# Kernel optimization log

Measured on AMD Instinct MI355X. Metric: run time of the kernel, lower is better.

## Reference

```python
import jax, jax.numpy as jnp
import numpy as np

HIDDEN = 64
FORECAST = 30
B, T = 4096, 1024


def setup_inputs() -> dict:
    key = jax.random.key(0)
    ks = jax.random.split(key, 7)
    s = 1.0 / np.sqrt(HIDDEN)  # torch LSTM/Linear uniform init scale
    u = lambda k, shape: jax.random.uniform(k, shape, jnp.float32, -s, s)
    return {
        "x": jax.random.normal(ks[0], (B, T, 1), jnp.float32),
        "W_ih": u(ks[1], (4 * HIDDEN, 1)),      # gates order: i, f, g, o (torch)
        "W_hh": u(ks[2], (4 * HIDDEN, HIDDEN)),
        "b_ih": u(ks[3], (4 * HIDDEN,)),
        "b_hh": u(ks[4], (4 * HIDDEN,)),
        "fc_W": u(ks[5], (FORECAST, HIDDEN)),
        "fc_b": u(ks[6], (FORECAST,)),
    }


def _lstm_last_hidden(x, W_ih, W_hh, b_ih, b_hh):
    # Precompute input contributions for all timesteps: [B, T, 4H]
    xg = jnp.einsum("bti,gi->btg", x, W_ih) + b_ih + b_hh
    H = W_hh.shape[1]
    W_hh_T = W_hh.T  # [H, 4H]

    def step(carry, xt):  # xt: [B, 4H]
        h, c = carry
        gates = xt + h @ W_hh_T
        i, f, g, o = jnp.split(gates, 4, axis=-1)
        i = jax.nn.sigmoid(i)
        f = jax.nn.sigmoid(f)
        g = jnp.tanh(g)
        o = jax.nn.sigmoid(o)
        c = f * c + i * g
        h = o * jnp.tanh(c)
        return (h, c), None

    Bsz = x.shape[0]
    h0 = jnp.zeros((Bsz, H), x.dtype)
    c0 = jnp.zeros((Bsz, H), x.dtype)
    (h_last, _), _ = jax.lax.scan(step, (h0, c0), jnp.swapaxes(xg, 0, 1))
    return h_last  # [B, H]


def reference(x, W_ih, W_hh, b_ih, b_hh, fc_W, fc_b):
    h_last = _lstm_last_hidden(x, W_ih, W_hh, b_ih, b_hh)
    return h_last @ fc_W.T + fc_b  # [B, FORECAST]
```

## Files before the change

kernel.cpp:

```cpp
#include <hip/hip_runtime.h>
#include <math.h>

#define T_STEPS 1024
#define FORECAST 30

typedef __attribute__((ext_vector_type(8))) _Float16 half8;
typedef __attribute__((ext_vector_type(2))) _Float16 half2v;
typedef __attribute__((ext_vector_type(4))) float f32x4;
typedef __attribute__((ext_vector_type(2))) float f32x2;

__device__ __forceinline__ float rcp_fast(float v){ return __builtin_amdgcn_rcpf(v); }
__device__ __forceinline__ float exp2_fast(float v){ return __builtin_amdgcn_exp2f(v); }
__device__ __forceinline__ f32x4 mfma16(half8 a, half8 b, f32x4 c){
    return __builtin_amdgcn_mfma_f32_16x16x32_f16(a, b, c, 0, 0, 0);
}
__device__ __forceinline__ half2v pack_f16(float a, float b){
    return __builtin_bit_cast(half2v, __builtin_amdgcn_cvt_pkrtz(a, b));
}

__global__ __launch_bounds__(512, 1)
void lstm_mfma_kernel(const float* __restrict__ x,
                      const float* __restrict__ W_ih,
                      const float* __restrict__ W_hh,
                      const float* __restrict__ b_ih,
                      const float* __restrict__ b_hh,
                      const float* __restrict__ fc_W,
                      const float* __restrict__ fc_b,
                      float* __restrict__ out)
{
    __shared__ __align__(16) _Float16 hs[2][16][64];
    __shared__ float xs[2][64][16];

    const int tid = threadIdx.x;
    const int l   = tid & 63;
    const int w   = tid >> 6;
    const int l15 = l & 15;
    const int l4  = l >> 4;
    const int bb  = blockIdx.x * 16;

    const float L2E  = 1.44269504088896f;
    const float TL2E = 2.88539008177793f;

    const int   ga   = l15 & 3;
    const float Srow = (ga == 2) ? TL2E : -L2E;
    half8 A[2][2];
    #pragma unroll
    for (int T = 0; T < 2; ++T) {
        const int gc = ga*64 + w*8 + T*4 + (l15 >> 2);
        #pragma unroll
        for (int kc = 0; kc < 2; ++kc) {
            #pragma unroll
            for (int e = 0; e < 8; ++e) {
                const int p   = kc*32 + l4*8 + e;
                const int jin = (p & ~7) + ((p & 1) << 2) + ((p & 7) >> 1);
                A[T][kc][e] = (_Float16)(W_hh[gc*64 + jin] * Srow);
            }
        }
    }

    float wih[2][4], bia[2][4];
    #pragma unroll
    for (int T = 0; T < 2; ++T) {
        const int jT = w*8 + T*4 + l4;
        #pragma unroll
        for (int r = 0; r < 4; ++r) {
            const float S = (r == 2) ? TL2E : -L2E;
            const int   g = r*64 + jT;
            wih[T][r] = W_ih[g] * S;
            bia[T][r] = (b_ih[g] + b_hh[g]) * S;
        }
    }

    const int rbase = (l15*128 + l4*16) ^ ((l15&7)<<4);
    const int hwoff = (l15*128 + w*16 + l4*4) ^ ((l15&7)<<4);
    char* const buf0 = (char*)hs;
    char* const buf1 = (char*)hs + 2048;

    #pragma unroll
    for (int it = 0; it < 2; ++it) {
        const int b = w*2 + it;
        xs[0][l][b] = x[(long long)(bb + b)*T_STEPS + l];
    }
    ((unsigned*)hs)[512 + tid] = 0u;
    __syncthreads();

    f32x2 cc = {0.f, 0.f}, hh01 = {0.f, 0.f};
    float xv = xs[0][0][l15];

    #define LSTM_STEP(T_CUR, RBUF, WBUF)                                        \
    {                                                                           \
        const int t_ = (T_CUR);                                                 \
        const half8 b0 = *(const half8*)((RBUF) + rbase);                       \
        const half8 b1 = *(const half8*)((RBUF) + (rbase ^ 64));                \
        f32x4 acc0, acc1;                                                       \
        _Pragma("unroll")                                                       \
        for (int r = 0; r < 4; ++r) {                                           \
            acc0[r] = fmaf(xv, wih[0][r], bia[0][r]);                           \
            acc1[r] = fmaf(xv, wih[1][r], bia[1][r]);                           \
        }                                                                       \
        acc0 = mfma16(A[0][0], b0, acc0);                                       \
        acc1 = mfma16(A[1][0], b0, acc1);                                       \
        acc0 = mfma16(A[0][1], b1, acc0);                                       \
        acc1 = mfma16(A[1][1], b1, acc1);                                       \
        const int t1_ = t_ + 1;                                                 \
        const float xvn = xs[(t1_ >> 6) & 1][t1_ & 63][l15];                    \
        f32x2 eI, eF, eG, eO;                                                   \
        eI[0] = exp2_fast(acc0[0]); eI[1] = exp2_fast(acc1[0]);                 \
        eF[0] = exp2_fast(acc0[1]); eF[1] = exp2_fast(acc1[1]);                 \
        eG[0] = exp2_fast(acc0[2]); eG[1] = exp2_fast(acc1[2]);                 \
        eO[0] = exp2_fast(acc0[3]); eO[1] = exp2_fast(acc1[3]);                 \
        const f32x2 u  = eI + 1.0f;                                             \
        const f32x2 v  = eF + 1.0f;                                             \
        const f32x2 s  = eG + 1.0f;                                             \
        const f32x2 m  = s - 2.0f;                                              \
        const f32x2 us = u * s;                                                 \
        const f32x2 vm = v * m;                                                 \
        const f32x2 N  = cc * us + vm;                                          \
        const f32x2 Dd = us * v;                                                \
        f32x2 rD; rD[0] = rcp_fast(Dd[0]); rD[1] = rcp_fast(Dd[1]);             \
        cc = N * rD;                                                            \
        f32x2 a2 = cc * TL2E;                                                   \
        a2[0] = fminf(a2[0], 80.f); a2[1] = fminf(a2[1], 80.f);                 \
        const f32x2 oD = eO + 1.0f;                                             \
        f32x2 Tt; Tt[0] = exp2_fast(a2[0]); Tt[1] = exp2_fast(a2[1]);           \
        const f32x2 Dh = oD * (Tt + 1.0f);                                      \
        f32x2 rH; rH[0] = rcp_fast(Dh[0]); rH[1] = rcp_fast(Dh[1]);             \
        hh01 = (Tt - 1.0f) * rH;                                                \
        *(half2v*)((WBUF) + hwoff) = pack_f16(hh01[0], hh01[1]);                \
        xv = xvn;                                                               \
        __syncthreads();                                                        \
    }

    for (int t2 = 0; t2 < T_STEPS; t2 += 2) {
        if ((t2 & 63) == 0 && t2 + 64 < T_STEPS) {
            #pragma unroll
            for (int it = 0; it < 2; ++it) {
                const int b = w*2 + it;
                xs[(((t2 >> 6) & 1)) ^ 1][l][b] =
                    x[(long long)(bb + b)*T_STEPS + t2 + 64 + l];
            }
        }
        LSTM_STEP(t2,     buf1, buf0);
        LSTM_STEP(t2 + 1, buf0, buf1);
    }
    #undef LSTM_STEP

    float* hsc = (float*)xs;
    hsc[l15*64 + w*8 + l4]     = hh01[0];
    hsc[l15*64 + w*8 + 4 + l4] = hh01[1];
    __syncthreads();

    if (tid < 16*FORECAST) {
        const int b = tid / FORECAST;
        const int f = tid % FORECAST;
        float a = fc_b[f];
        #pragma unroll
        for (int jj = 0; jj < 64; ++jj)
            a = fmaf(hsc[b*64 + jj], fc_W[f*64 + jj], a);
        out[(long long)(bb + b)*FORECAST + f] = a;
    }
}

extern "C" void kernel_launch(void* const* d_in, const int* in_sizes, int n_in,
                              void* d_out, int out_size, void* d_ws, size_t ws_size,
                              hipStream_t stream) {
    const float* x    = (const float*)d_in[0];
    const float* W_ih = (const float*)d_in[1];
    const float* W_hh = (const float*)d_in[2];
    const float* b_ih = (const float*)d_in[3];
    const float* b_hh = (const float*)d_in[4];
    const float* fc_W = (const float*)d_in[5];
    const float* fc_b = (const float*)d_in[6];
    float* out = (float*)d_out;

    lstm_mfma_kernel<<<256, 512, 0, stream>>>(x, W_ih, W_hh, b_ih, b_hh, fc_W, fc_b, out);
}
```

Before: 371.1 us.

## Halve batch per block, spread gate math across lanes, use rational tanh

```diff
diff --git a/kernel.cpp b/kernel.cpp
--- a/kernel.cpp
+++ b/kernel.cpp
@@ -3,22 +3,19 @@
 
 #define T_STEPS 1024
 #define FORECAST 30
+#define BPB 8
 
 typedef __attribute__((ext_vector_type(8))) _Float16 half8;
-typedef __attribute__((ext_vector_type(2))) _Float16 half2v;
 typedef __attribute__((ext_vector_type(4))) float f32x4;
-typedef __attribute__((ext_vector_type(2))) float f32x2;
 
 __device__ __forceinline__ float rcp_fast(float v){ return __builtin_amdgcn_rcpf(v); }
 __device__ __forceinline__ float exp2_fast(float v){ return __builtin_amdgcn_exp2f(v); }
+__device__ __forceinline__ float med3(float a, float lo, float hi){ return __builtin_amdgcn_fmed3f(a, lo, hi); }
 __device__ __forceinline__ f32x4 mfma16(half8 a, half8 b, f32x4 c){
     return __builtin_amdgcn_mfma_f32_16x16x32_f16(a, b, c, 0, 0, 0);
 }
-__device__ __forceinline__ half2v pack_f16(float a, float b){
-    return __builtin_bit_cast(half2v, __builtin_amdgcn_cvt_pkrtz(a, b));
-}
 
-__global__ __launch_bounds__(512, 1)
+__global__ __launch_bounds__(512, 4)
 void lstm_mfma_kernel(const float* __restrict__ x,
                       const float* __restrict__ W_ih,
                       const float* __restrict__ W_hh,
@@ -28,15 +25,17 @@
                       const float* __restrict__ fc_b,
                       float* __restrict__ out)
 {
-    __shared__ __align__(16) _Float16 hs[2][16][64];
-    __shared__ float xs[2][64][16];
+    __shared__ __align__(16) _Float16 hs[2][BPB][64];
+    __shared__ float xs[2][64][BPB];
 
     const int tid = threadIdx.x;
     const int l   = tid & 63;
     const int w   = tid >> 6;
     const int l15 = l & 15;
     const int l4  = l >> 4;
-    const int bb  = blockIdx.x * 16;
+    const int b7  = l15 & 7;
+    const int sel = l15 >> 3;
+    const int bb  = blockIdx.x * BPB;
 
     const float L2E  = 1.44269504088896f;
     const float TL2E = 2.88539008177793f;
@@ -49,12 +48,10 @@
         const int gc = ga*64 + w*8 + T*4 + (l15 >> 2);
         #pragma unroll
         for (int kc = 0; kc < 2; ++kc) {
+            const float* p = W_hh + gc*64 + kc*32 + l4*8;
             #pragma unroll
-            for (int e = 0; e < 8; ++e) {
-                const int p   = kc*32 + l4*8 + e;
-                const int jin = (p & ~7) + ((p & 1) << 2) + ((p & 7) >> 1);
-                A[T][kc][e] = (_Float16)(W_hh[gc*64 + jin] * Srow);
-            }
+            for (int e = 0; e < 8; ++e)
+                A[T][kc][e] = (_Float16)(p[e] * Srow);
         }
     }
 
@@ -71,21 +68,18 @@
         }
     }
 
-    const int rbase = (l15*128 + l4*16) ^ ((l15&7)<<4);
-    const int hwoff = (l15*128 + w*16 + l4*4) ^ ((l15&7)<<4);
+    const int rbase = (b7*128 + l4*16) ^ (b7<<4);
+    const int jk    = w*8 + sel*4 + l4;
+    const int hwoff = (b7*128 + jk*2) ^ (b7<<4);
     char* const buf0 = (char*)hs;
-    char* const buf1 = (char*)hs + 2048;
+    char* const buf1 = (char*)hs + 1024;
 
-    #pragma unroll
-    for (int it = 0; it < 2; ++it) {
-        const int b = w*2 + it;
-        xs[0][l][b] = x[(long long)(bb + b)*T_STEPS + l];
-    }
-    ((unsigned*)hs)[512 + tid] = 0u;
+    xs[0][l][w] = x[(long long)(bb + w)*T_STEPS + l];
+    if (tid < 256) ((unsigned*)hs)[256 + tid] = 0u;
     __syncthreads();
 
-    f32x2 cc = {0.f, 0.f}, hh01 = {0.f, 0.f};
-    float xv = xs[0][0][l15];
+    float cc = 0.f, hh = 0.f;
+    float xv = xs[0][0][b7];
 
     #define LSTM_STEP(T_CUR, RBUF, WBUF)                                        \
     {                                                                           \
@@ -103,54 +97,50 @@
         acc0 = mfma16(A[0][1], b1, acc0);                                       \
         acc1 = mfma16(A[1][1], b1, acc1);                                       \
         const int t1_ = t_ + 1;                                                 \
-        const float xvn = xs[(t1_ >> 6) & 1][t1_ & 63][l15];                    \
-        f32x2 eI, eF, eG, eO;                                                   \
-        eI[0] = exp2_fast(acc0[0]); eI[1] = exp2_fast(acc1[0]);                 \
-        eF[0] = exp2_fast(acc0[1]); eF[1] = exp2_fast(acc1[1]);                 \
-        eG[0] = exp2_fast(acc0[2]); eG[1] = exp2_fast(acc1[2]);                 \
-        eO[0] = exp2_fast(acc0[3]); eO[1] = exp2_fast(acc1[3]);                 \
-        const f32x2 u  = eI + 1.0f;                                             \
-        const f32x2 v  = eF + 1.0f;                                             \
-        const f32x2 s  = eG + 1.0f;                                             \
-        const f32x2 m  = s - 2.0f;                                              \
-        const f32x2 us = u * s;                                                 \
-        const f32x2 vm = v * m;                                                 \
-        const f32x2 N  = cc * us + vm;                                          \
-        const f32x2 Dd = us * v;                                                \
-        f32x2 rD; rD[0] = rcp_fast(Dd[0]); rD[1] = rcp_fast(Dd[1]);             \
-        cc = N * rD;                                                            \
-        f32x2 a2 = cc * TL2E;                                                   \
-        a2[0] = fminf(a2[0], 80.f); a2[1] = fminf(a2[1], 80.f);                 \
-        const f32x2 oD = eO + 1.0f;                                             \
-        f32x2 Tt; Tt[0] = exp2_fast(a2[0]); Tt[1] = exp2_fast(a2[1]);           \
-        const f32x2 Dh = oD * (Tt + 1.0f);                                      \
-        f32x2 rH; rH[0] = rcp_fast(Dh[0]); rH[1] = rcp_fast(Dh[1]);             \
-        hh01 = (Tt - 1.0f) * rH;                                                \
-        *(half2v*)((WBUF) + hwoff) = pack_f16(hh01[0], hh01[1]);                \
+        const float xvn = xs[(t1_ >> 6) & 1][t1_ & 63][b7];                     \
+        f32x4 a;                                                                \
+        _Pragma("unroll")                                                       \
+        for (int r = 0; r < 4; ++r) a[r] = sel ? acc1[r] : acc0[r];             \
+        const float eI = exp2_fast(a[0]);                                       \
+        const float eF = exp2_fast(a[1]);                                       \
+        const float eG = exp2_fast(a[2]);                                       \
+        const float eO = exp2_fast(a[3]);                                       \
+        const float u  = 1.0f + eI;                                             \
+        const float v  = 1.0f + eF;                                             \
+        const float s  = 1.0f + eG;                                             \
+        const float m  = s - 2.0f;                                              \
+        const float us = u * s;                                                 \
+        const float N  = fmaf(cc, us, v * m);                                   \
+        cc = N * rcp_fast(us * v);                         \
+        const float ct = med3(cc, -4.6f, 4.6f);                                 \
+        const float z  = ct * ct;                                               \
+        float q = fmaf(z, 21.0f, 1260.0f);                                      \
+        q = fmaf(z, q, 10395.0f);                                               \
+        const float Pn = ct * q;                                                \
+        float r_ = z + 210.0f;                                                  \
+        r_ = fmaf(z, r_, 4725.0f);                                              \
+        r_ = fmaf(z, r_, 10395.0f);                                             \
+        const float Dh = (eO + 1.0f) * r_;                \
+        hh = Pn * rcp_fast(Dh);                            \
+        *(_Float16*)((WBUF) + hwoff) = (_Float16)hh;                            \
         xv = xvn;                                                               \
         __syncthreads();                                                        \
     }
 
     for (int t2 = 0; t2 < T_STEPS; t2 += 2) {
-        if ((t2 & 63) == 0 && t2 + 64 < T_STEPS) {
-            #pragma unroll
-            for (int it = 0; it < 2; ++it) {
-                const int b = w*2 + it;
-                xs[(((t2 >> 6) & 1)) ^ 1][l][b] =
-                    x[(long long)(bb + b)*T_STEPS + t2 + 64 + l];
-            }
-        }
+        if ((t2 & 63) == 0 && t2 + 64 < T_STEPS)
+            xs[((t2 >> 6) & 1) ^ 1][l][w] =
+                x[(long long)(bb + w)*T_STEPS + t2 + 64 + l];
         LSTM_STEP(t2,     buf1, buf0);
         LSTM_STEP(t2 + 1, buf0, buf1);
     }
     #undef LSTM_STEP
 
     float* hsc = (float*)xs;
-    hsc[l15*64 + w*8 + l4]     = hh01[0];
-    hsc[l15*64 + w*8 + 4 + l4] = hh01[1];
+    hsc[b7*64 + jk] = hh;
     __syncthreads();
 
-    if (tid < 16*FORECAST) {
+    if (tid < BPB*FORECAST) {
         const int b = tid / FORECAST;
         const int f = tid % FORECAST;
         float a = fc_b[f];
@@ -173,5 +163,5 @@
     const float* fc_b = (const float*)d_in[6];
     float* out = (float*)d_out;
 
-    lstm_mfma_kernel<<<256, 512, 0, stream>>>(x, W_ih, W_hh, b_ih, b_hh, fc_W, fc_b, out);
+    lstm_mfma_kernel<<<512, 512, 0, stream>>>(x, W_ih, W_hh, b_ih, b_hh, fc_W, fc_b, out);
 }
```

Measured after the change: 493.6 us. +33.0%, slower.
